# Kernel optimization log

Measured on AMD Instinct MI355X. Metric: run time of the kernel, lower is better.

The kernel has to match this reference:

```python
import jax, jax.numpy as jnp
import numpy as np

NUM_HEADS = 16
MAX_LEN = 2048


def setup_inputs() -> dict:
    key = jax.random.key(0)
    ks = jax.random.split(key, 10)
    L, B, C = 2048, 2, 1024
    s = 0.02
    return {
        "x": jax.random.normal(ks[0], (L, B, C), dtype=jnp.float32),
        "Wq": jax.random.normal(ks[1], (C, C), dtype=jnp.float32) * s,
        "bq": jnp.zeros((C,), dtype=jnp.float32),
        "Wk": jax.random.normal(ks[2], (C, C), dtype=jnp.float32) * s,
        "bk": jnp.zeros((C,), dtype=jnp.float32),
        "Wv": jax.random.normal(ks[3], (C, C), dtype=jnp.float32) * s,
        "bv": jnp.zeros((C,), dtype=jnp.float32),
        "Wo": jax.random.normal(ks[4], (C, C), dtype=jnp.float32) * s,
        "bo": jnp.zeros((C,), dtype=jnp.float32),
        "rel": jax.random.normal(ks[5], (2 * MAX_LEN - 1,), dtype=jnp.float32) * s,
    }


def reference(x, Wq, bq, Wk, bk, Wv, bv, Wo, bo, rel):
    L, B, C = x.shape
    H = NUM_HEADS
    hd = C // H
    scale = hd ** (-0.5)
    xb = jnp.transpose(x, (1, 0, 2))  # (B, L, C)

    def heads(y):  # (B, L, C) -> (B, H, L, hd)
        return jnp.transpose(y.reshape(B, L, H, hd), (0, 2, 1, 3))

    Q = heads(xb @ Wq + bq)
    K = heads(xb @ Wk + bk)
    V = heads(xb @ Wv + bv)

    scores = jnp.einsum("bhqd,bhkd->bhqk", Q, K)  # (B, H, L, L)
    # relative-position bias gather: offset = k - q + max_len - 1
    idx = jnp.arange(L)[None, :] - jnp.arange(L)[:, None] + (MAX_LEN - 1)
    R = rel[idx]  # (L, L)
    scores = (scores + R[None, None, :, :]) * scale
    w = jax.nn.softmax(scores, axis=-1)
    attn = jnp.einsum("bhqk,bhkd->bhqd", w, V)  # (B, H, L, hd)
    attn = jnp.transpose(attn, (0, 2, 1, 3)).reshape(B, L, C)
    attn = jnp.transpose(attn, (1, 0, 2))  # (L, B, C)
    return attn @ Wo + bo
```

## Files before the change

### kernel.cpp

```cpp
#include <hip/hip_runtime.h>

#define L_SEQ 2048
#define BATCH 2
#define CDIM  1024
#define NH    16
#define HD    64

typedef __attribute__((ext_vector_type(8))) short short8;
typedef __attribute__((ext_vector_type(4))) float floatx4;

#define QSCALE 0.18033688011112042f

__device__ __forceinline__ unsigned short f2bf(float f){
  unsigned int u = __builtin_bit_cast(unsigned int, f);
  u += 0x7fffu + ((u >> 16) & 1u);
  return (unsigned short)(u >> 16);
}

__device__ __forceinline__ unsigned cvtpk(float lo, float hi){
  unsigned r;
  asm("v_cvt_pk_bf16_f32 %0, %1, %2" : "=v"(r) : "v"(lo), "v"(hi));
  return r;
}

__device__ __forceinline__ void gload_lds16(const void* g, void* l){
  typedef __attribute__((address_space(1))) void gv_t;
  typedef __attribute__((address_space(3))) void sv_t;
  __builtin_amdgcn_global_load_lds((gv_t*)(void*)g, (sv_t*)l, 16, 0, 0);
}

__global__ void __launch_bounds__(256) prep_x(const float* __restrict__ x,
                                              unsigned short* __restrict__ xb){
  int idx = blockIdx.x * 256 + threadIdx.x;
  int c4 = idx & 255;
  int lb = idx >> 8;
  int b  = lb & (BATCH - 1);
  int l  = lb >> 1;
  float4 v = ((const float4*)x)[idx];
  ushort4 s;
  s.x = f2bf(v.x); s.y = f2bf(v.y); s.z = f2bf(v.z); s.w = f2bf(v.w);
  *(ushort4*)&xb[(size_t)(b*L_SEQ + l)*CDIM + c4*4] = s;
}

__global__ void __launch_bounds__(256) prep_w(const float* __restrict__ Wq,
    const float* __restrict__ Wk, const float* __restrict__ Wv,
    const float* __restrict__ Wo, unsigned short* __restrict__ Wqkvt,
    unsigned short* __restrict__ Wot){
  __shared__ float tile[32][33];
  int z = blockIdx.z;
  const float* W = (z==0)?Wq:(z==1)?Wk:(z==2)?Wv:Wo;
  unsigned short* dst = (z==3) ? Wot : (Wqkvt + (size_t)z*CDIM*CDIM);
  int tx = threadIdx.x & 31, ty = threadIdx.x >> 5;
  int X = blockIdx.x*32, Y = blockIdx.y*32;
  #pragma unroll
  for (int i=0;i<4;i++)
    tile[ty + i*8][tx] = W[(size_t)(Y + ty + i*8)*CDIM + X + tx];
  __syncthreads();
  #pragma unroll
  for (int i=0;i<4;i++)
    dst[(size_t)(X + ty + i*8)*CDIM + Y + tx] = f2bf(tile[tx][ty + i*8]);
}

template<int MODE>
__global__ void __launch_bounds__(256) gemm_bt(
    const unsigned short* __restrict__ A,
    const unsigned short* __restrict__ Bt,
    int Kdim,
    const float* __restrict__ b0, const float* __restrict__ b1,
    const float* __restrict__ b2,
    unsigned short* __restrict__ qo, unsigned short* __restrict__ ko,
    unsigned short* __restrict__ vo, float* __restrict__ out)
{
  __shared__ unsigned short Asm[128*32];
  __shared__ unsigned short Bsm[128*32];
  const int t    = threadIdx.x;
  const int lane = t & 63;
  const int wave = t >> 6;
  const int wr = wave >> 1, wc = wave & 1;
  const int g = lane >> 4, lr = lane & 15;
  const int rowA0 = blockIdx.x * 128;
  const int rowB0 = blockIdx.y * 128;

  floatx4 acc[4][4] = {};

  const int r_st = t >> 2;
  const int k_st = (t & 3) * 8;

  for (int k0 = 0; k0 < Kdim; k0 += 32) {
    const unsigned short* ga = A  + (size_t)(rowA0 + r_st) * Kdim + k0 + k_st;
    const unsigned short* gb = Bt + (size_t)(rowB0 + r_st) * Kdim + k0 + k_st;
    gload_lds16(ga,                   &Asm[t*8]);
    gload_lds16(ga + (size_t)64*Kdim, &Asm[2048 + t*8]);
    gload_lds16(gb,                   &Bsm[t*8]);
    gload_lds16(gb + (size_t)64*Kdim, &Bsm[2048 + t*8]);
    __syncthreads();
    short8 af[4], bfr[4];
    #pragma unroll
    for (int mi=0;mi<4;mi++)
      af[mi] = *(const short8*)&Asm[(wr*64 + mi*16 + lr)*32 + g*8];
    #pragma unroll
    for (int ni=0;ni<4;ni++)
      bfr[ni] = *(const short8*)&Bsm[(wc*64 + ni*16 + lr)*32 + g*8];
    #pragma unroll
    for (int mi=0;mi<4;mi++)
      #pragma unroll
      for (int ni=0;ni<4;ni++)
        acc[mi][ni] = __builtin_amdgcn_mfma_f32_16x16x32_bf16(af[mi], bfr[ni], acc[mi][ni], 0, 0, 0);
    __syncthreads();
  }

  #pragma unroll
  for (int mi=0;mi<4;mi++){
    const int rb = rowA0 + wr*64 + mi*16 + g*4;
    #pragma unroll
    for (int ni=0;ni<4;ni++){
      const int col = rowB0 + wc*64 + ni*16 + lr;
      if (MODE == 0) {
        const int sec = col >> 10;
        const int nl  = col & 1023;
        const int h = nl >> 6, d = nl & 63;
        const float* bp = (sec==0) ? b0 : (sec==1) ? b1 : b2;
        const float bias = bp[nl];
        #pragma unroll
        for (int r=0;r<4;r++){
          const int row = rb + r;
          const int b = row >> 11, l = row & 2047;
          float v = acc[mi][ni][r] + bias;
          if (sec == 0) v *= QSCALE;
          const unsigned short hv = f2bf(v);
          const size_t bh = (size_t)(b*NH + h);
          if (sec == 0)      qo[(bh*L_SEQ + l)*HD + d] = hv;
          else if (sec == 1) ko[(bh*L_SEQ + l)*HD + d] = hv;
          else               vo[(bh*HD + d)*L_SEQ + l] = hv;
        }
      } else {
        const float bias = b0[col];
        #pragma unroll
        for (int r=0;r<4;r++){
          const int row = rb + r;
          const int b = row >> 11, l = row & 2047;
          out[((size_t)l*BATCH + b)*CDIM + col] = acc[mi][ni][r] + bias;
        }
      }
    }
  }
}

__global__ void __launch_bounds__(256) attn_kernel(
    const unsigned short* __restrict__ Qb, const unsigned short* __restrict__ Kb,
    const unsigned short* __restrict__ Vt, const float* __restrict__ rel,
    unsigned short* __restrict__ Ab)
{
  __shared__ unsigned short Ks[2][64*64];
  __shared__ unsigned short Vs[2][64*64];
  __shared__ unsigned int Pl[4*16*32];
  const int bh = blockIdx.x;
  const int qb = blockIdx.y;
  const int t = threadIdx.x, lane = t & 63, wave = t >> 6;
  const int g = lane >> 4, lr = lane & 15;

  const unsigned short* Qp = Qb + (size_t)bh * (L_SEQ*HD);
  const unsigned short* Kp = Kb + (size_t)bh * (L_SEQ*HD);
  const unsigned short* Vp = Vt + (size_t)bh * (HD*L_SEQ);

  const int q0 = qb*64 + wave*16;
  const short8 qf0 = *(const short8*)&Qp[(size_t)(q0 + lr)*HD + g*8];
  const short8 qf1 = *(const short8*)&Qp[(size_t)(q0 + lr)*HD + 32 + g*8];

  const float* relp = rel + (2047 - q0 - lr + g*4);

  unsigned int* pw = Pl + wave*512 + lr*32;
  const int swz = lr & 7;

  const short ONE = (short)0x3F80;
  const short8 ones = { ONE,ONE,ONE,ONE,ONE,ONE,ONE,ONE };

  const int srow = t >> 3;
  const int sxor = (t & 7) ^ (srow & 7);

  const unsigned short* kg = Kp + (size_t)srow*HD + sxor*8;
  const unsigned short* vg = Vp + (size_t)srow*L_SEQ + sxor*8;

  floatx4 o[4] = {};
  floatx4 osum = {};
  float m = -1e30f;

  gload_lds16(kg,           &Ks[0][t*8]);
  gload_lds16(kg + 32*HD,   &Ks[0][2048 + t*8]);
  gload_lds16(vg,           &Vs[0][t*8]);
  gload_lds16(vg + (size_t)32*L_SEQ, &Vs[0][2048 + t*8]);
  __syncthreads();

  int cur = 0;
  for (int kb = 0; kb < L_SEQ; kb += 64) {
    {
      const int kbn = (kb + 64) & (L_SEQ - 1);
      const unsigned short* kgn = kg + (size_t)kbn*HD;
      const unsigned short* vgn = vg + kbn;
      unsigned short* kd = &Ks[cur^1][0];
      unsigned short* vd = &Vs[cur^1][0];
      gload_lds16(kgn,                    kd + t*8);
      gload_lds16(kgn + 32*HD,            kd + 2048 + t*8);
      gload_lds16(vgn,                    vd + t*8);
      gload_lds16(vgn + (size_t)32*L_SEQ, vd + 2048 + t*8);
    }

    float relv[16];
    #pragma unroll
    for (int j=0;j<4;j++)
      #pragma unroll
      for (int r=0;r<4;r++)
        relv[4*j+r] = relp[kb + 16*j + r];

    const unsigned short* kbuf = &Ks[cur][0];
    floatx4 s[4];
    #pragma unroll
    for (int j=0;j<4;j++){
      const int row = j*16 + lr;
      const short8 k0 = *(const short8*)&kbuf[row*64 + ((g    ) ^ swz)*8];
      const short8 k1 = *(const short8*)&kbuf[row*64 + ((4 + g) ^ swz)*8];
      floatx4 z = {};
      z = __builtin_amdgcn_mfma_f32_16x16x32_bf16(k0, qf0, z, 0,0,0);
      z = __builtin_amdgcn_mfma_f32_16x16x32_bf16(k1, qf1, z, 0,0,0);
      s[j] = z;
    }

    float p[16];
    #pragma unroll
    for (int j=0;j<4;j++)
      #pragma unroll
      for (int r=0;r<4;r++)
        p[4*j+r] = fmaf(relv[4*j+r], QSCALE, s[j][r]);

    float ma = fmaxf(fmaxf(fmaxf(p[0],p[1]),p[2]),  fmaxf(fmaxf(p[3],p[4]),p[5]));
    float mb = fmaxf(fmaxf(fmaxf(p[6],p[7]),p[8]),  fmaxf(fmaxf(p[9],p[10]),p[11]));
    float mc = fmaxf(fmaxf(fmaxf(p[12],p[13]),p[14]), p[15]);
    float mxl = fmaxf(fmaxf(ma, mb), mc);

    if (!__all(mxl <= m + 8.f)) {
      float mx = fmaxf(mxl, __shfl_xor(mxl, 16, 64));
      mx = fmaxf(mx, __shfl_xor(mx, 32, 64));
      const float mn = fmaxf(m, mx);
      const float al = exp2f(m - mn);
      m = mn;
      #pragma unroll
      for (int r=0;r<4;r++) osum[r] *= al;
      #pragma unroll
      for (int fb=0;fb<4;fb++)
        #pragma unroll
        for (int r=0;r<4;r++) o[fb][r] *= al;
    }

    #pragma unroll
    for (int i=0;i<16;i++) p[i] = exp2f(p[i] - m);

    #pragma unroll
    for (int j=0;j<4;j++){
      unsigned lo = cvtpk(p[4*j],   p[4*j+1]);
      unsigned hi = cvtpk(p[4*j+2], p[4*j+3]);
      const int unit = (2*j + (g>>1)) ^ swz;
      *(uint2*)&pw[unit*4 + (g&1)*2] = make_uint2(lo, hi);
    }
    asm volatile("" ::: "memory");
    const short8 pf0 = *(const short8*)&pw[((    g) ^ swz)*4];
    const short8 pf1 = *(const short8*)&pw[((4 + g) ^ swz)*4];
    asm volatile("" ::: "memory");

    osum = __builtin_amdgcn_mfma_f32_16x16x32_bf16(ones, pf0, osum, 0,0,0);
    osum = __builtin_amdgcn_mfma_f32_16x16x32_bf16(ones, pf1, osum, 0,0,0);

    const unsigned short* vbuf = &Vs[cur][0];
    #pragma unroll
    for (int fb=0; fb<4; fb++){
      const int row = fb*16 + lr;
      const short8 v0 = *(const short8*)&vbuf[row*64 + ((g    ) ^ swz)*8];
      const short8 v1 = *(const short8*)&vbuf[row*64 + ((4 + g) ^ swz)*8];
      o[fb] = __builtin_amdgcn_mfma_f32_16x16x32_bf16(v0, pf0, o[fb], 0,0,0);
      o[fb] = __builtin_amdgcn_mfma_f32_16x16x32_bf16(v1, pf1, o[fb], 0,0,0);
    }

    __syncthreads();
    cur ^= 1;
  }

  const float inv = 1.f / osum[0];
  const int b = bh >> 4, h = bh & 15;
  unsigned short* outp = &Ab[((size_t)(b*L_SEQ + q0 + lr))*CDIM + h*HD];
  #pragma unroll
  for (int fb=0; fb<4; fb++){
    #pragma unroll
    for (int rp=0; rp<2; rp++){
      *(unsigned int*)&outp[fb*16 + g*4 + 2*rp] =
          cvtpk(o[fb][2*rp] * inv, o[fb][2*rp+1] * inv);
    }
  }
}

extern "C" void kernel_launch(void* const* d_in, const int* in_sizes, int n_in,
                              void* d_out, int out_size, void* d_ws, size_t ws_size,
                              hipStream_t stream) {
  const float* x   = (const float*)d_in[0];
  const float* Wq  = (const float*)d_in[1];
  const float* bq  = (const float*)d_in[2];
  const float* Wk  = (const float*)d_in[3];
  const float* bk  = (const float*)d_in[4];
  const float* Wv  = (const float*)d_in[5];
  const float* bv  = (const float*)d_in[6];
  const float* Wo  = (const float*)d_in[7];
  const float* bo  = (const float*)d_in[8];
  const float* rel = (const float*)d_in[9];
  float* out = (float*)d_out;

  char* ws = (char*)d_ws;
  unsigned short* Xb    = (unsigned short*)(ws);
  unsigned short* Wqkvt = (unsigned short*)(ws + (8u  << 20));
  unsigned short* Wot   = (unsigned short*)(ws + (14u << 20));
  unsigned short* Qb    = (unsigned short*)(ws + (16u << 20));
  unsigned short* Kb    = (unsigned short*)(ws + (24u << 20));
  unsigned short* Vt    = (unsigned short*)(ws + (32u << 20));
  unsigned short* Ab    = Xb;

  prep_x<<<4096, 256, 0, stream>>>(x, Xb);
  prep_w<<<dim3(32,32,4), 256, 0, stream>>>(Wq, Wk, Wv, Wo, Wqkvt, Wot);
  gemm_bt<0><<<dim3(32,24), 256, 0, stream>>>(Xb, Wqkvt, CDIM, bq, bk, bv,
                                              Qb, Kb, Vt, nullptr);
  attn_kernel<<<dim3(32,32), 256, 0, stream>>>(Qb, Kb, Vt, rel, Ab);
  gemm_bt<1><<<dim3(32,8), 256, 0, stream>>>(Ab, Wot, CDIM, bo, nullptr, nullptr,
                                             nullptr, nullptr, nullptr, out);
}
```

Baseline: 240.3 us.

## Stage V projection tile through LDS for coalesced transposed writes; relax attention barriers

In the QKV projection GEMM, blocks that produce the V section now convert their accumulators to bf16, write them transposed into shared memory, and then emit coalesced 16-byte stores into the transposed V layout. This replaces the scattered 2-byte stores that used to be strided by L_SEQ. The attention loop also swaps the full __syncthreads for an explicit vmcnt(4) wait plus a raw barrier, so the prefetch of the next K/V tile can stay in flight while the current tile is consumed. The hand-written waitcnt counts are a correctness risk, and the larger LDS footprint in MODE 0 may lower occupancy.

Measured after the change: 248.7 us. 3.5% more time.

```diff
diff --git a/kernel.cpp b/kernel.cpp
--- a/kernel.cpp
+++ b/kernel.cpp
@@ -71,8 +71,11 @@
     unsigned short* __restrict__ qo, unsigned short* __restrict__ ko,
     unsigned short* __restrict__ vo, float* __restrict__ out)
 {
-  __shared__ unsigned short Asm[128*32];
-  __shared__ unsigned short Bsm[128*32];
+  constexpr int SMEM_HW = (MODE==0) ? 16896 : 8192;
+  __shared__ __align__(16) unsigned short smem[SMEM_HW];
+  unsigned short* Asm = &smem[0];
+  unsigned short* Bsm = &smem[4096];
+  unsigned short* Vb  = &smem[0];
   const int t    = threadIdx.x;
   const int lane = t & 63;
   const int wave = t >> 6;
@@ -109,6 +112,33 @@
     __syncthreads();
   }
 
+  if (MODE==0 && rowB0 >= 2048) {
+    #pragma unroll
+    for (int mi=0;mi<4;mi++){
+      const int rloc = wr*64 + mi*16 + g*4;
+      #pragma unroll
+      for (int ni=0;ni<4;ni++){
+        const int cloc = wc*64 + ni*16 + lr;
+        const float bias = b2[(rowB0 + cloc) & 1023];
+        const unsigned u0 = cvtpk(acc[mi][ni][0]+bias, acc[mi][ni][1]+bias);
+        const unsigned u1 = cvtpk(acc[mi][ni][2]+bias, acc[mi][ni][3]+bias);
+        *(uint2*)&Vb[cloc*132 + rloc] = make_uint2(u0, u1);
+      }
+    }
+    __syncthreads();
+    const int dloc = t >> 1, half = t & 1;
+    const int nl = (rowB0 + dloc) & 1023;
+    const int h = nl >> 6, d = nl & 63;
+    const int b = rowA0 >> 11;
+    const int l0 = (rowA0 & 2047) + half*64;
+    unsigned short* dst = &vo[((size_t)((b*NH + h)*HD + d))*L_SEQ + l0];
+    const unsigned short* srcp = &Vb[dloc*132 + half*64];
+    #pragma unroll
+    for (int i=0;i<8;i++)
+      *(short8*)&dst[i*8] = *(const short8*)&srcp[i*8];
+    return;
+  }
+
   #pragma unroll
   for (int mi=0;mi<4;mi++){
     const int rb = rowA0 + wr*64 + mi*16 + g*4;
@@ -119,8 +149,7 @@
         const int sec = col >> 10;
         const int nl  = col & 1023;
         const int h = nl >> 6, d = nl & 63;
-        const float* bp = (sec==0) ? b0 : (sec==1) ? b1 : b2;
-        const float bias = bp[nl];
+        const float bias = (sec==0) ? b0[nl] : b1[nl];
         #pragma unroll
         for (int r=0;r<4;r++){
           const int row = rb + r;
@@ -129,9 +158,8 @@
           if (sec == 0) v *= QSCALE;
           const unsigned short hv = f2bf(v);
           const size_t bh = (size_t)(b*NH + h);
-          if (sec == 0)      qo[(bh*L_SEQ + l)*HD + d] = hv;
-          else if (sec == 1) ko[(bh*L_SEQ + l)*HD + d] = hv;
-          else               vo[(bh*HD + d)*L_SEQ + l] = hv;
+          if (sec == 0) qo[(bh*L_SEQ + l)*HD + d] = hv;
+          else          ko[(bh*L_SEQ + l)*HD + d] = hv;
         }
       } else {
         const float bias = b0[col];
@@ -189,7 +217,6 @@
   gload_lds16(kg + 32*HD,   &Ks[0][2048 + t*8]);
   gload_lds16(vg,           &Vs[0][t*8]);
   gload_lds16(vg + (size_t)32*L_SEQ, &Vs[0][2048 + t*8]);
-  __syncthreads();
 
   int cur = 0;
   for (int kb = 0; kb < L_SEQ; kb += 64) {
@@ -204,6 +231,8 @@
       gload_lds16(vgn,                    vd + t*8);
       gload_lds16(vgn + (size_t)32*L_SEQ, vd + 2048 + t*8);
     }
+    asm volatile("s_waitcnt vmcnt(4)" ::: "memory");
+    __builtin_amdgcn_s_barrier();
 
     float relv[16];
     #pragma unroll
@@ -279,7 +308,7 @@
       o[fb] = __builtin_amdgcn_mfma_f32_16x16x32_bf16(v1, pf1, o[fb], 0,0,0);
     }
 
-    __syncthreads();
+    __builtin_amdgcn_s_barrier();
     cur ^= 1;
   }
 
```

## Double-buffer GEMM LDS loads and use partial vmcnt waits in GEMM and attention

Applied to the files above, without the earlier changes.

The projection GEMM now double-buffers its A/B tiles in LDS, issuing the next k-tile's global-to-LDS loads before computing on the current one. Both GEMM and attention replace full __syncthreads with an s_waitcnt vmcnt(4) plus a raw barrier, so the newest prefetch can stay in flight. The QKV epilogue also stores V transposed as packed 4-element vectors and hoists the row index math. The risks are relying on vmcnt counting for correctness, a wasted wraparound prefetch on the last iteration, and twice the LDS per GEMM block, which may lower occupancy.

New measurement: 229.8 us. -4.4%, faster.

```diff
diff --git a/kernel.cpp b/kernel.cpp
--- a/kernel.cpp
+++ b/kernel.cpp
@@ -71,8 +71,7 @@
     unsigned short* __restrict__ qo, unsigned short* __restrict__ ko,
     unsigned short* __restrict__ vo, float* __restrict__ out)
 {
-  __shared__ unsigned short Asm[128*32];
-  __shared__ unsigned short Bsm[128*32];
+  __shared__ __align__(16) unsigned short smem[16384];
   const int t    = threadIdx.x;
   const int lane = t & 63;
   const int wave = t >> 6;
@@ -86,32 +85,49 @@
   const int r_st = t >> 2;
   const int k_st = (t & 3) * 8;
 
+  const unsigned short* ga0 = A  + (size_t)(rowA0 + r_st) * Kdim + k_st;
+  const unsigned short* gb0 = Bt + (size_t)(rowB0 + r_st) * Kdim + k_st;
+
+  gload_lds16(ga0,                   &smem[t*8]);
+  gload_lds16(ga0 + (size_t)64*Kdim, &smem[2048 + t*8]);
+  gload_lds16(gb0,                   &smem[4096 + t*8]);
+  gload_lds16(gb0 + (size_t)64*Kdim, &smem[4096 + 2048 + t*8]);
+
+  int cur = 0;
   for (int k0 = 0; k0 < Kdim; k0 += 32) {
-    const unsigned short* ga = A  + (size_t)(rowA0 + r_st) * Kdim + k0 + k_st;
-    const unsigned short* gb = Bt + (size_t)(rowB0 + r_st) * Kdim + k0 + k_st;
-    gload_lds16(ga,                   &Asm[t*8]);
-    gload_lds16(ga + (size_t)64*Kdim, &Asm[2048 + t*8]);
-    gload_lds16(gb,                   &Bsm[t*8]);
-    gload_lds16(gb + (size_t)64*Kdim, &Bsm[2048 + t*8]);
-    __syncthreads();
+    {
+      const int k1 = (k0 + 32) & (Kdim - 1);
+      unsigned short* nb = &smem[(cur^1)*8192];
+      gload_lds16(ga0 + k1,                   nb + t*8);
+      gload_lds16(ga0 + k1 + (size_t)64*Kdim, nb + 2048 + t*8);
+      gload_lds16(gb0 + k1,                   nb + 4096 + t*8);
+      gload_lds16(gb0 + k1 + (size_t)64*Kdim, nb + 4096 + 2048 + t*8);
+    }
+    asm volatile("s_waitcnt vmcnt(4)" ::: "memory");
+    __builtin_amdgcn_s_barrier();
+
+    const unsigned short* cb = &smem[cur*8192];
     short8 af[4], bfr[4];
     #pragma unroll
     for (int mi=0;mi<4;mi++)
-      af[mi] = *(const short8*)&Asm[(wr*64 + mi*16 + lr)*32 + g*8];
+      af[mi] = *(const short8*)&cb[(wr*64 + mi*16 + lr)*32 + g*8];
     #pragma unroll
     for (int ni=0;ni<4;ni++)
-      bfr[ni] = *(const short8*)&Bsm[(wc*64 + ni*16 + lr)*32 + g*8];
+      bfr[ni] = *(const short8*)&cb[4096 + (wc*64 + ni*16 + lr)*32 + g*8];
     #pragma unroll
     for (int mi=0;mi<4;mi++)
       #pragma unroll
       for (int ni=0;ni<4;ni++)
         acc[mi][ni] = __builtin_amdgcn_mfma_f32_16x16x32_bf16(af[mi], bfr[ni], acc[mi][ni], 0, 0, 0);
-    __syncthreads();
+
+    __builtin_amdgcn_s_barrier();
+    cur ^= 1;
   }
 
   #pragma unroll
   for (int mi=0;mi<4;mi++){
     const int rb = rowA0 + wr*64 + mi*16 + g*4;
+    const int b  = rb >> 11, l0 = rb & 2047;
     #pragma unroll
     for (int ni=0;ni<4;ni++){
       const int col = rowB0 + wc*64 + ni*16 + lr;
@@ -119,28 +135,29 @@
         const int sec = col >> 10;
         const int nl  = col & 1023;
         const int h = nl >> 6, d = nl & 63;
-        const float* bp = (sec==0) ? b0 : (sec==1) ? b1 : b2;
-        const float bias = bp[nl];
-        #pragma unroll
-        for (int r=0;r<4;r++){
-          const int row = rb + r;
-          const int b = row >> 11, l = row & 2047;
-          float v = acc[mi][ni][r] + bias;
-          if (sec == 0) v *= QSCALE;
-          const unsigned short hv = f2bf(v);
-          const size_t bh = (size_t)(b*NH + h);
-          if (sec == 0)      qo[(bh*L_SEQ + l)*HD + d] = hv;
-          else if (sec == 1) ko[(bh*L_SEQ + l)*HD + d] = hv;
-          else               vo[(bh*HD + d)*L_SEQ + l] = hv;
+        const size_t bh = (size_t)(b*NH + h);
+        if (sec == 2) {
+          const float bias = b2[nl];
+          ushort4 s;
+          s.x = f2bf(acc[mi][ni][0]+bias); s.y = f2bf(acc[mi][ni][1]+bias);
+          s.z = f2bf(acc[mi][ni][2]+bias); s.w = f2bf(acc[mi][ni][3]+bias);
+          *(ushort4*)&vo[(bh*HD + d)*L_SEQ + l0] = s;
+        } else {
+          const float bias = (sec==0) ? b0[nl] : b1[nl];
+          #pragma unroll
+          for (int r=0;r<4;r++){
+            float v = acc[mi][ni][r] + bias;
+            if (sec == 0) v *= QSCALE;
+            const unsigned short hv = f2bf(v);
+            if (sec == 0) qo[(bh*L_SEQ + l0 + r)*HD + d] = hv;
+            else          ko[(bh*L_SEQ + l0 + r)*HD + d] = hv;
+          }
         }
       } else {
         const float bias = b0[col];
         #pragma unroll
-        for (int r=0;r<4;r++){
-          const int row = rb + r;
-          const int b = row >> 11, l = row & 2047;
-          out[((size_t)l*BATCH + b)*CDIM + col] = acc[mi][ni][r] + bias;
-        }
+        for (int r=0;r<4;r++)
+          out[((size_t)(l0 + r)*BATCH + b)*CDIM + col] = acc[mi][ni][r] + bias;
       }
     }
   }
@@ -189,7 +206,6 @@
   gload_lds16(kg + 32*HD,   &Ks[0][2048 + t*8]);
   gload_lds16(vg,           &Vs[0][t*8]);
   gload_lds16(vg + (size_t)32*L_SEQ, &Vs[0][2048 + t*8]);
-  __syncthreads();
 
   int cur = 0;
   for (int kb = 0; kb < L_SEQ; kb += 64) {
@@ -204,6 +220,8 @@
       gload_lds16(vgn,                    vd + t*8);
       gload_lds16(vgn + (size_t)32*L_SEQ, vd + 2048 + t*8);
     }
+    asm volatile("s_waitcnt vmcnt(4)" ::: "memory");
+    __builtin_amdgcn_s_barrier();
 
     float relv[16];
     #pragma unroll
@@ -279,7 +297,7 @@
       o[fb] = __builtin_amdgcn_mfma_f32_16x16x32_bf16(v1, pf1, o[fb], 0,0,0);
     }
 
-    __syncthreads();
+    __builtin_amdgcn_s_barrier();
     cur ^= 1;
   }
 
```
